# Optimization experiments

Hardware: AMD Instinct MI355X
Metric: run time of the kernel (lower is better)

Reference implementation:

```python
import jax, jax.numpy as jnp
import numpy as np

BINS = 10
MOMENTUM = 0.5
N = 16_777_216  # flat element / class count


def setup_inputs() -> dict:
    key = jax.random.key(0)
    k1, k2 = jax.random.split(key)
    pred = jax.random.normal(k1, (N,), dtype=jnp.float32)
    target = jax.random.uniform(k2, (N,), dtype=jnp.float32)
    return {"pred": pred, "target": target}


def reference(pred, target):
    # edges = linspace(0,1,bins+1) with last edge nudged up by 1e-6
    edges = jnp.linspace(0.0, 1.0, BINS + 1).at[-1].add(1e-6)

    # gradient magnitude g = |sigmoid(pred).detach() - target|
    p_sig = jax.lax.stop_gradient(jax.nn.sigmoid(pred))
    g = jnp.abs(p_sig - target)

    valid = jnp.isfinite(g) & jnp.isfinite(target)
    total_samples = jnp.sum(valid).astype(jnp.float32)

    # torch.bucketize(g, edges) with right=False == searchsorted left
    inds = jnp.searchsorted(edges, g, side="left")  # values in [0, BINS]
    # bincount(inds, minlength=BINS) -> histogram over BINS+1 buckets,
    # counting only valid elements (scatter-add)
    sample_in_bin = jnp.zeros(BINS + 1, jnp.float32).at[inds].add(
        valid.astype(jnp.float32)
    )

    # EMA: stored acc_sum is never updated in the torch module (stays zeros),
    # so the local acc_sum = momentum*0 + (1-momentum)*counts each call.
    acc_sum_state = jnp.zeros(BINS + 1, jnp.float32)
    acc_sum = MOMENTUM * acc_sum_state + (1.0 - MOMENTUM) * sample_in_bin

    total_positives = jnp.sum(acc_sum)
    total_negatives = total_samples - total_positives  # computed pre-clamp
    total_positives = jnp.maximum(total_positives, 1.0)

    pred_det = jax.lax.stop_gradient(pred)
    ratio = total_negatives / total_positives
    weights = jnp.where(target > pred_det, ratio, 1.0)
    weights = jnp.where(valid, weights, 0.0)  # weights only defined on valid

    # F.cross_entropy with 1-D logits [C], float (soft-label) target [C],
    # per-class weight [C], reduction='mean' on a single unbatched sample:
    # loss = -sum_c w_c * t_c * log_softmax(pred)_c
    logp = jax.nn.log_softmax(pred)
    loss = -jnp.sum(weights * target * logp)
    return loss
```

## Files before the change

### kernel.cpp

```cpp
#include <hip/hip_runtime.h>
#include <math.h>


#define NT 256
#define NB 2048
#define UN 4
#define SHIFTC 16.0f

__device__ __forceinline__ float min4(float4 t) { return fminf(fminf(t.x, t.y), fminf(t.z, t.w)); }
__device__ __forceinline__ float max4(float4 t) { return fmaxf(fmaxf(t.x, t.y), fmaxf(t.z, t.w)); }

struct Acc5 { float S, At, Bt, Agt, Bgt; };

__device__ __forceinline__ void acc_elem(Acc5& a, float p, float t) {
    const float L2E = 1.4426950408889634f;
    a.S += exp2f(fmaf(p, L2E, -SHIFTC));
    float ts = (t > p) ? t : 0.0f;
    a.Bt += t;
    a.Bgt += ts;
    a.At  = fmaf(t,  p, a.At);
    a.Agt = fmaf(ts, p, a.Agt);
}

__device__ __forceinline__ void acc_group(Acc5& a, float4 p, float4 t) {
    acc_elem(a, p.x, t.x); acc_elem(a, p.y, t.y);
    acc_elem(a, p.z, t.z); acc_elem(a, p.w, t.w);
}

__device__ __forceinline__ void hist_fix(float& hd, float p, float t) {
    const float L2E = 1.4426950408889634f;
    if (isfinite(t)) {
        float sig = 1.0f / (1.0f + exp2f(-p * L2E));
        float g = fabsf(sig - t);
        if (g > 1.000001f) hd += 1.0f;
    }
}

__device__ __forceinline__ void fix_group(float& hd, float4 p, float4 t) {
    hist_fix(hd, p.x, t.x); hist_fix(hd, p.y, t.y);
    hist_fix(hd, p.z, t.z); hist_fix(hd, p.w, t.w);
}

__device__ __forceinline__ void proc_group(Acc5& a, float& hd, float4 P, float4 T) {
    acc_group(a, P, T);
    if (!(min4(T) >= 0.0f && max4(T) <= 1.0f)) fix_group(hd, P, T);
}

__device__ __forceinline__ void block_reduce_write(float* v, float* out8) {
    #pragma unroll
    for (int off = 32; off > 0; off >>= 1) {
        #pragma unroll
        for (int q = 0; q < 6; q++) v[q] += __shfl_down(v[q], off);
    }
    __shared__ float red[NT / 64][6];
    int wave = threadIdx.x >> 6;
    int lane = threadIdx.x & 63;
    if (lane == 0) {
        #pragma unroll
        for (int q = 0; q < 6; q++) red[wave][q] = v[q];
    }
    __syncthreads();
    if (threadIdx.x == 0) {
        float s[6];
        #pragma unroll
        for (int q = 0; q < 6; q++) s[q] = red[0][q];
        #pragma unroll
        for (int w = 1; w < NT / 64; w++)
            #pragma unroll
            for (int q = 0; q < 6; q++) s[q] += red[w][q];
        #pragma unroll
        for (int q = 0; q < 6; q++) out8[q] = s[q];
    }
}

__global__ __launch_bounds__(NT) void ghm_pass1(const float* __restrict__ pred,
                                                const float* __restrict__ targ,
                                                float* __restrict__ ws, int n) {
    const float4* p4 = (const float4*)pred;
    const float4* t4 = (const float4*)targ;
    int tid = blockIdx.x * NT + threadIdx.x;
    int nth = gridDim.x * NT;
    int n4 = n >> 2;

    Acc5 acc[UN];
    #pragma unroll
    for (int u = 0; u < UN; u++) acc[u] = {0.f, 0.f, 0.f, 0.f, 0.f};
    float hd = 0.0f;

    int iters = n4 / nth;
    int i = tid;
    int k = 0;
    for (; k + UN <= iters; k += UN) {
        float4 P[UN], T[UN];
        #pragma unroll
        for (int u = 0; u < UN; u++) P[u] = p4[i + u * nth];
        #pragma unroll
        for (int u = 0; u < UN; u++) T[u] = t4[i + u * nth];
        #pragma unroll
        for (int u = 0; u < UN; u++) proc_group(acc[u], hd, P[u], T[u]);
        i += UN * nth;
    }
    for (; k < iters; k++) {
        proc_group(acc[0], hd, p4[i], t4[i]);
        i += nth;
    }
    for (int j = iters * nth + tid; j < n4; j += nth)
        proc_group(acc[0], hd, p4[j], t4[j]);
    if (tid == 0) {
        for (int j = n4 << 2; j < n; j++) {
            acc_elem(acc[0], pred[j], targ[j]);
            float t = targ[j];
            if (!(t >= 0.0f && t <= 1.0f)) hist_fix(hd, pred[j], t);
        }
    }

    #pragma unroll
    for (int u = 1; u < UN; u++) {
        acc[0].S += acc[u].S;   acc[0].At  += acc[u].At;
        acc[0].Bt += acc[u].Bt; acc[0].Agt += acc[u].Agt;
        acc[0].Bgt += acc[u].Bgt;
    }
    float v[6] = {acc[0].S, acc[0].At, acc[0].Bt, acc[0].Agt, acc[0].Bgt, hd};
    block_reduce_write(v, &ws[(size_t)blockIdx.x * 8]);
}

__global__ __launch_bounds__(NT) void ghm_pass2(const float* __restrict__ ws,
                                                float* __restrict__ out, int nb, int n) {
    float v[6] = {0.f, 0.f, 0.f, 0.f, 0.f, 0.f};
    for (int i = threadIdx.x; i < nb; i += NT) {
        const float* p = &ws[(size_t)i * 8];
        #pragma unroll
        for (int q = 0; q < 6; q++) v[q] += p[q];
    }
    __shared__ float res[8];
    block_reduce_write(v, res);
    if (threadIdx.x == 0) {
        float S = res[0], At = res[1], Bt = res[2], Agt = res[3], Bgt = res[4], hd = res[5];
        float cnt  = (float)n;
        float hcnt = cnt - hd;
        float tp0  = 0.5f * hcnt;
        float tneg = cnt - tp0;
        float ratio = tneg / fmaxf(tp0, 1.0f);
        float A = ratio * Agt + (At - Agt);
        float B = ratio * Bgt + (Bt - Bgt);
        float lse = (log2f(S) + SHIFTC) * 0.69314718055994531f;
        out[0] = lse * B - A;
    }
}

extern "C" void kernel_launch(void* const* d_in, const int* in_sizes, int n_in,
                              void* d_out, int out_size, void* d_ws, size_t ws_size,
                              hipStream_t stream) {
    const float* pred = (const float*)d_in[0];
    const float* targ = (const float*)d_in[1];
    float* out = (float*)d_out;
    float* ws = (float*)d_ws;
    int n = in_sizes[0];

    int nb = NB;
    size_t need = (size_t)nb * 8 * sizeof(float);
    if (ws_size < need) {
        nb = (int)(ws_size / (8 * sizeof(float)));
        if (nb < 1) nb = 1;
    }

    ghm_pass1<<<nb, NT, 0, stream>>>(pred, targ, ws, n);
    ghm_pass2<<<1, NT, 0, stream>>>(ws, out, nb, n);
}
```

Measured before the change: 149.8 us.

## Switch pass1 to block-contiguous chunked grid-stride and raise grid to 4096 blocks

Each block now processes contiguous chunks of NT*UN float4s per iteration, instead of strided whole-grid interleaving, and keeps a single accumulator rather than UN separate ones. The grid grows from 2048 to up to 4096 blocks. The goal is better DRAM locality per block and more memory-level parallelism on a bandwidth-bound streaming reduction. The single accumulator lengthens dependency chains and can change summation rounding.

After: 147.5 us. No clear change (-1.5%).

```diff
diff --git a/kernel.cpp b/kernel.cpp
--- a/kernel.cpp
+++ b/kernel.cpp
@@ -3,8 +3,9 @@
 
 
 #define NT 256
-#define NB 2048
 #define UN 4
+#define CHUNK_F4 (NT * UN)
+#define MAXNB 4096
 #define SHIFTC 16.0f
 
 __device__ __forceinline__ float min4(float4 t) { return fminf(fminf(t.x, t.y), fminf(t.z, t.w)); }
@@ -75,52 +76,40 @@
 
 __global__ __launch_bounds__(NT) void ghm_pass1(const float* __restrict__ pred,
                                                 const float* __restrict__ targ,
-                                                float* __restrict__ ws, int n) {
+                                                float* __restrict__ ws,
+                                                int n, int nchunks) {
     const float4* p4 = (const float4*)pred;
     const float4* t4 = (const float4*)targ;
-    int tid = blockIdx.x * NT + threadIdx.x;
-    int nth = gridDim.x * NT;
+    int tid = threadIdx.x;
     int n4 = n >> 2;
 
-    Acc5 acc[UN];
-    #pragma unroll
-    for (int u = 0; u < UN; u++) acc[u] = {0.f, 0.f, 0.f, 0.f, 0.f};
+    Acc5 a = {0.f, 0.f, 0.f, 0.f, 0.f};
     float hd = 0.0f;
 
-    int iters = n4 / nth;
-    int i = tid;
-    int k = 0;
-    for (; k + UN <= iters; k += UN) {
+    for (int c = blockIdx.x; c < nchunks; c += gridDim.x) {
+        int base = c * CHUNK_F4 + tid;
         float4 P[UN], T[UN];
         #pragma unroll
-        for (int u = 0; u < UN; u++) P[u] = p4[i + u * nth];
+        for (int u = 0; u < UN; u++) P[u] = p4[base + u * NT];
         #pragma unroll
-        for (int u = 0; u < UN; u++) T[u] = t4[i + u * nth];
+        for (int u = 0; u < UN; u++) T[u] = t4[base + u * NT];
         #pragma unroll
-        for (int u = 0; u < UN; u++) proc_group(acc[u], hd, P[u], T[u]);
-        i += UN * nth;
+        for (int u = 0; u < UN; u++) proc_group(a, hd, P[u], T[u]);
     }
-    for (; k < iters; k++) {
-        proc_group(acc[0], hd, p4[i], t4[i]);
-        i += nth;
-    }
-    for (int j = iters * nth + tid; j < n4; j += nth)
-        proc_group(acc[0], hd, p4[j], t4[j]);
-    if (tid == 0) {
+
+    for (int j = nchunks * CHUNK_F4 + blockIdx.x * NT + tid; j < n4;
+         j += gridDim.x * NT)
+        proc_group(a, hd, p4[j], t4[j]);
+
+    if (blockIdx.x == 0 && tid == 0) {
         for (int j = n4 << 2; j < n; j++) {
-            acc_elem(acc[0], pred[j], targ[j]);
-            float t = targ[j];
-            if (!(t >= 0.0f && t <= 1.0f)) hist_fix(hd, pred[j], t);
+            float p = pred[j], t = targ[j];
+            acc_elem(a, p, t);
+            if (!(t >= 0.0f && t <= 1.0f)) hist_fix(hd, p, t);
         }
     }
 
-    #pragma unroll
-    for (int u = 1; u < UN; u++) {
-        acc[0].S += acc[u].S;   acc[0].At  += acc[u].At;
-        acc[0].Bt += acc[u].Bt; acc[0].Agt += acc[u].Agt;
-        acc[0].Bgt += acc[u].Bgt;
-    }
-    float v[6] = {acc[0].S, acc[0].At, acc[0].Bt, acc[0].Agt, acc[0].Bgt, hd};
+    float v[6] = {a.S, a.At, a.Bt, a.Agt, a.Bgt, hd};
     block_reduce_write(v, &ws[(size_t)blockIdx.x * 8]);
 }
 
@@ -156,14 +145,14 @@
     float* out = (float*)d_out;
     float* ws = (float*)d_ws;
     int n = in_sizes[0];
+    int n4 = n >> 2;
+    int nchunks = n4 / CHUNK_F4;
 
-    int nb = NB;
-    size_t need = (size_t)nb * 8 * sizeof(float);
-    if (ws_size < need) {
-        nb = (int)(ws_size / (8 * sizeof(float)));
-        if (nb < 1) nb = 1;
-    }
+    int nb = nchunks < MAXNB ? (nchunks > 0 ? nchunks : 1) : MAXNB;
+    size_t cap = ws_size / (8 * sizeof(float));
+    if ((size_t)nb > cap) nb = (int)cap;
+    if (nb < 1) nb = 1;
 
-    ghm_pass1<<<nb, NT, 0, stream>>>(pred, targ, ws, n);
+    ghm_pass1<<<nb, NT, 0, stream>>>(pred, targ, ws, n, nchunks);
     ghm_pass2<<<1, NT, 0, stream>>>(ws, out, nb, n);
 }
```
